# Kernel optimization log

Measured on AMD Instinct MI355X. Metric: run time of the kernel, lower is better.

The kernel has to match this reference:

```python
import jax, jax.numpy as jnp
import numpy as np

B, C, T = 8, 512, 2048
G = 32          # GroupNorm groups
HEADS = 8       # C // head_channels(64)
EPS = 1e-5


def setup_inputs() -> dict:
    key = jax.random.key(0)
    ks = jax.random.split(key, 7)
    s = 0.02
    return {
        "x": jax.random.normal(ks[0], (B, C, T), dtype=jnp.float32),
        "gn_w": jnp.ones((C,), dtype=jnp.float32),
        "gn_b": jnp.zeros((C,), dtype=jnp.float32),
        "qkv_w": jax.random.normal(ks[1], (3 * C, C), dtype=jnp.float32) * s,
        "qkv_b": jnp.zeros((3 * C,), dtype=jnp.float32),
        "proj_w": jax.random.normal(ks[2], (C, C), dtype=jnp.float32) * s,
        "proj_b": jnp.zeros((C,), dtype=jnp.float32),
    }


def reference(x, gn_w, gn_b, qkv_w, qkv_b, proj_w, proj_b):
    b, c, t = x.shape
    ch = c // HEADS
    # GroupNorm(32, C): normalize over (channels-in-group, T)
    xg = x.reshape(b, G, (c // G) * t)
    mu = jnp.mean(xg, axis=-1, keepdims=True)
    var = jnp.var(xg, axis=-1, keepdims=True)
    h = ((xg - mu) * jax.lax.rsqrt(var + EPS)).reshape(b, c, t)
    h = h * gn_w[:, None] + gn_b[:, None]
    # 1x1 Conv1d -> pointwise linear over channels
    qkv = jnp.einsum('oc,bct->bot', qkv_w, h) + qkv_b[:, None]  # [b, 3c, t]
    q, k, v = jnp.split(qkv, 3, axis=1)
    scale = ch ** -0.25
    q = (q * scale).reshape(b * HEADS, ch, t)
    k = (k * scale).reshape(b * HEADS, ch, t)
    v = v.reshape(b * HEADS, ch, t)
    w = jnp.einsum('bct,bcs->bts', q, k)  # [b*H, t, t]
    w = jax.nn.softmax(w.astype(jnp.float32), axis=-1).astype(q.dtype)
    a = jnp.einsum('bts,bcs->bct', w, v).reshape(b, c, t)
    out = jnp.einsum('oc,bct->bot', proj_w, a) + proj_b[:, None]
    return x + out
```

## Files before the change

kernel.cpp:

```cpp
#include <hip/hip_runtime.h>
#include <hip/hip_bf16.h>
#include <math.h>

#define NB 8
#define NC 512
#define NT 2048
#define NG 32
#define NH 8
#define CH 64

typedef __attribute__((ext_vector_type(8))) short short8;
typedef __attribute__((ext_vector_type(4))) short short4v;
typedef __attribute__((ext_vector_type(4))) float floatx4;

static __device__ __forceinline__ short f2bf(float f) {
    __hip_bfloat16 h = __float2bfloat16(f);
    return *reinterpret_cast<short*>(&h);
}

static __device__ __forceinline__ int pk2bf_trunc(float lo, float hi) {
    return (int)__builtin_amdgcn_perm(__builtin_bit_cast(unsigned, hi),
                                      __builtin_bit_cast(unsigned, lo),
                                      0x07060302u);
}

static __device__ __forceinline__ void gload_lds16(const short* g, short* l) {
    __builtin_amdgcn_global_load_lds(
        (const __attribute__((address_space(1))) void*)g,
        (__attribute__((address_space(3))) void*)l, 16, 0, 0);
}

__global__ __launch_bounds__(256) void castw_kernel(
    const float* __restrict__ qw, const float* __restrict__ pw,
    short* __restrict__ qo, short* __restrict__ po)
{
    const int i = blockIdx.x * 256 + threadIdx.x;
    const bool isq = i < 196608;
    const int j = isq ? i : i - 196608;
    float4 v = isq ? ((const float4*)qw)[j] : ((const float4*)pw)[j];
    short4v s;
    s.x = f2bf(v.x); s.y = f2bf(v.y); s.z = f2bf(v.z); s.w = f2bf(v.w);
    if (isq) *(short4v*)&qo[j * 4] = s;
    else     *(short4v*)&po[j * 4] = s;
}

__global__ __launch_bounds__(256) void gn_stats_kernel(
    const float* __restrict__ x, float* __restrict__ stats)
{
    __shared__ float red[16];
    const int tid = threadIdx.x;
    const int grp = blockIdx.x;
    const float4* xp = (const float4*)(x + (size_t)grp * 16 * NT);

    float s = 0.f, ss = 0.f;
    for (int i = tid; i < 8192; i += 256) {
        float4 v = xp[i];
        s  += v.x + v.y + v.z + v.w;
        ss += v.x*v.x + v.y*v.y + v.z*v.z + v.w*v.w;
    }
    #pragma unroll
    for (int o = 32; o > 0; o >>= 1) {
        s  += __shfl_down(s,  o, 64);
        ss += __shfl_down(ss, o, 64);
    }
    const int lane = tid & 63, wid = tid >> 6;
    if (lane == 0) { red[wid] = s; red[8 + wid] = ss; }
    __syncthreads();
    if (tid == 0) {
        const float inv = 1.f / 32768.f;
        const float mean = (red[0] + red[1] + red[2] + red[3]) * inv;
        const float var  = (red[8] + red[9] + red[10] + red[11]) * inv - mean * mean;
        stats[grp * 2]     = mean;
        stats[grp * 2 + 1] = rsqrtf(var + 1e-5f);
    }
}

__global__ __launch_bounds__(256) void gn_apply_kernel(
    const float* __restrict__ x, const float* __restrict__ gw,
    const float* __restrict__ gb, const float* __restrict__ stats,
    short* __restrict__ ht)
{
    __shared__ float wc_s[NC], bc_s[NC];
    __shared__ float tile[64 * 68];
    const int tid = threadIdx.x;
    const int b = blockIdx.y;
    const int t0 = blockIdx.x * 64;

    for (int c = tid; c < NC; c += 256) {
        const int g = c >> 4;
        const float mean = stats[(b * NG + g) * 2];
        const float rstd = stats[(b * NG + g) * 2 + 1];
        const float wc = gw[c] * rstd;
        wc_s[c] = wc;
        bc_s[c] = gb[c] - mean * wc;
    }

    const int cl = tid >> 2;
    const int k4 = tid & 3;
    const int tl = tid >> 2;
    const int cs = (tid & 3) * 16;

    for (int p = 0; p < 8; ++p) {
        const int c0 = p * 64;
        __syncthreads();
        const float* src = x + ((size_t)b * NC + c0 + cl) * NT + t0;
        #pragma unroll
        for (int k = 0; k < 4; ++k) {
            float4 v = *(const float4*)(src + k4 * 16 + k * 4);
            *(float4*)&tile[cl * 68 + k4 * 16 + k * 4] = v;
        }
        __syncthreads();
        short v16[16];
        #pragma unroll
        for (int j = 0; j < 16; ++j) {
            const int c = c0 + cs + j;
            v16[j] = f2bf(tile[(cs + j) * 68 + tl] * wc_s[c] + bc_s[c]);
        }
        short* dst = ht + ((size_t)b * NT + t0 + tl) * NC + c0 + cs;
        *(short8*)&dst[0] = *(const short8*)&v16[0];
        *(short8*)&dst[8] = *(const short8*)&v16[8];
    }
}

#define BK 32
__global__ __launch_bounds__(256) void qkv_gemm_kernel(
    const short* __restrict__ wb, const short* __restrict__ ht,
    const float* __restrict__ bias,
    short* __restrict__ q_t, short* __restrict__ k_t, short* __restrict__ vv)
{
    __shared__ short As[128 * BK];
    __shared__ short Bs[128 * BK];
    const int tid = threadIdx.x;
    const int wv = tid >> 6, lane = tid & 63;
    const int l16 = lane & 15, quad = lane >> 4;
    const int n0 = blockIdx.x * 128;
    const int m0 = blockIdx.y * 128;
    const int wm = wv & 1, wn = wv >> 1;

    floatx4 acc[4][4];
    #pragma unroll
    for (int i = 0; i < 4; ++i)
        #pragma unroll
        for (int j = 0; j < 4; ++j) acc[i][j] = (floatx4){0.f, 0.f, 0.f, 0.f};

    const short* gsrc = (wv < 2) ? wb : ht;
    const int rbase = (wv & 1) * 64;
    const int tile0 = (wv < 2) ? m0 : n0;
    short* lbuf = (wv < 2) ? As : Bs;
    const int lrow = lane >> 2;
    const int lcol = (lane & 3) * 8;

    for (int k0 = 0; k0 < 512; k0 += BK) {
        __syncthreads();
        #pragma unroll
        for (int ch = 0; ch < 4; ++ch) {
            const int row = rbase + ch * 16 + lrow;
            gload_lds16(gsrc + (size_t)(tile0 + row) * 512 + k0 + lcol,
                        lbuf + (rbase + ch * 16) * BK);
        }
        __syncthreads();

        short8 af[4], bfr[4];
        #pragma unroll
        for (int i = 0; i < 4; ++i) {
            af[i]  = *(const short8*)&As[(wm * 64 + i * 16 + l16) * BK + quad * 8];
            bfr[i] = *(const short8*)&Bs[(wn * 64 + i * 16 + l16) * BK + quad * 8];
        }
        #pragma unroll
        for (int i = 0; i < 4; ++i)
            #pragma unroll
            for (int j = 0; j < 4; ++j)
                acc[i][j] = __builtin_amdgcn_mfma_f32_16x16x32_bf16(
                    af[i], bfr[j], acc[i][j], 0, 0, 0);
    }

    const float kscale = 0.35355339059327373f;
    const float qscale = 0.35355339059327373f * 1.4426950408889634f;
    #pragma unroll
    for (int i = 0; i < 4; ++i) {
        const int o16 = m0 + wm * 64 + i * 16;
        const int sel = o16 >> 9;
        const int hh  = (o16 >> 6) & 7;
        const int c16 = o16 & 63;
        const float4 b4 = *(const float4*)&bias[o16 + quad * 4];
        const float sc = (sel == 0) ? qscale : kscale;
        #pragma unroll
        for (int j = 0; j < 4; ++j) {
            const int tg = n0 + wn * 64 + j * 16 + l16;
            const int b = tg >> 11, t = tg & 2047;
            floatx4 v = acc[i][j];
            v[0] += b4.x; v[1] += b4.y; v[2] += b4.z; v[3] += b4.w;
            if (sel < 2) {
                short4v s;
                s.x = f2bf(v[0] * sc); s.y = f2bf(v[1] * sc);
                s.z = f2bf(v[2] * sc); s.w = f2bf(v[3] * sc);
                short* dst = (sel == 0 ? q_t : k_t) +
                    (((size_t)(b * NH + hh) * NT + t) * CH + c16 + quad * 4);
                *(short4v*)dst = s;
            } else {
                short* dst = vv + ((size_t)(b * NH + hh) * CH + c16 + quad * 4) * NT + t;
                #pragma unroll
                for (int r = 0; r < 4; ++r) dst[(size_t)r * NT] = f2bf(v[r]);
            }
        }
    }
}

__global__ __launch_bounds__(512, 4) void attn_kernel(
    const short* __restrict__ qg, const short* __restrict__ kg,
    const short* __restrict__ vg, short* __restrict__ at)
{
    __shared__ short qps[256 * 64];
    __shared__ short kt[2][64 * 64];
    __shared__ short vs[2][64 * 64];

    const int tid = threadIdx.x;
    const int wv = tid >> 6, lane = tid & 63;
    const int l16 = lane & 15, quad = lane >> 4;
    const int xr = l16 & 7;
    const int t0 = blockIdx.x * 256;
    const int bh = blockIdx.y;
    const int b = bh >> 3, hd = bh & 7;
    const short* qh = qg + (size_t)bh * NT * CH;
    const short* kh = kg + (size_t)bh * NT * CH;
    const short* vh = vg + (size_t)bh * CH * NT;

    #pragma unroll
    for (int q = 0; q < 4; ++q) {
        const int F = (wv * 4 + q) * 64 + lane;
        const int row = F >> 3, cc = (F & 7) ^ (row & 7);
        gload_lds16(qh + (size_t)(t0 + row) * CH + cc * 8, &qps[(wv * 4 + q) * 512]);
    }
    {
        const int row = tid >> 3, cc = (tid & 7) ^ (row & 7);
        gload_lds16(kh + (size_t)row * CH + cc * 8, &kt[0][wv * 512]);
        gload_lds16(vh + (size_t)row * NT + cc * 8, &vs[0][wv * 512]);
    }
    __syncthreads();

    short8 bq[2][2];
    #pragma unroll
    for (int qt = 0; qt < 2; ++qt) {
        const int row = wv * 32 + qt * 16 + l16;
        #pragma unroll
        for (int ks = 0; ks < 2; ++ks) {
            const int c = (quad | (ks << 2)) ^ xr;
            bq[qt][ks] = *(const short8*)&qps[row * 64 + c * 8];
        }
    }

    floatx4 Oa[4][2];
    #pragma unroll
    for (int ct = 0; ct < 4; ++ct)
        #pragma unroll
        for (int qt = 0; qt < 2; ++qt) Oa[ct][qt] = (floatx4){0.f, 0.f, 0.f, 0.f};
    float l_part[2] = {0.f, 0.f};

    for (int it = 0; it < NT / 64; ++it) {
        __syncthreads();
        if (it + 1 < NT / 64) {
            const int s0n = (it + 1) * 64;
            const int row = tid >> 3, cc = (tid & 7) ^ (row & 7);
            gload_lds16(kh + (size_t)(s0n + row) * CH + cc * 8,
                        &kt[(it + 1) & 1][wv * 512]);
            gload_lds16(vh + (size_t)row * NT + s0n + cc * 8,
                        &vs[(it + 1) & 1][wv * 512]);
        }
        const short* kc = kt[it & 1];
        const short* vc = vs[it & 1];

        floatx4 sacc[4][2];
        #pragma unroll
        for (int nt = 0; nt < 4; ++nt)
            #pragma unroll
            for (int qt = 0; qt < 2; ++qt) sacc[nt][qt] = (floatx4){0.f, 0.f, 0.f, 0.f};
        #pragma unroll
        for (int ks = 0; ks < 2; ++ks) {
            const int c = (quad | (ks << 2)) ^ xr;
            #pragma unroll
            for (int nt = 0; nt < 4; ++nt) {
                short8 ak = *(const short8*)&kc[(nt * 16 + l16) * 64 + c * 8];
                #pragma unroll
                for (int qt = 0; qt < 2; ++qt)
                    sacc[nt][qt] = __builtin_amdgcn_mfma_f32_16x16x32_bf16(
                        ak, bq[qt][ks], sacc[nt][qt], 0, 0, 0);
            }
        }

        #pragma unroll
        for (int qt = 0; qt < 2; ++qt) {
            float sn[4];
            #pragma unroll
            for (int nt = 0; nt < 4; ++nt) {
                const float p0 = __builtin_amdgcn_exp2f(sacc[nt][qt][0]);
                const float p1 = __builtin_amdgcn_exp2f(sacc[nt][qt][1]);
                const float p2 = __builtin_amdgcn_exp2f(sacc[nt][qt][2]);
                const float p3 = __builtin_amdgcn_exp2f(sacc[nt][qt][3]);
                sacc[nt][qt][0] = p0; sacc[nt][qt][1] = p1;
                sacc[nt][qt][2] = p2; sacc[nt][qt][3] = p3;
                sn[nt] = (p0 + p1) + (p2 + p3);
            }
            l_part[qt] += (sn[0] + sn[1]) + (sn[2] + sn[3]);
        }

        #pragma unroll
        for (int qt = 0; qt < 2; ++qt) {
            const int row = wv * 32 + qt * 16 + l16;
            #pragma unroll
            for (int nt = 0; nt < 4; ++nt) {
                const int cw = (2 * nt + (quad >> 1)) ^ xr;
                int2 pv;
                pv.x = pk2bf_trunc(sacc[nt][qt][0], sacc[nt][qt][1]);
                pv.y = pk2bf_trunc(sacc[nt][qt][2], sacc[nt][qt][3]);
                *(int2*)&qps[row * 64 + cw * 8 + (quad & 1) * 4] = pv;
            }
        }

        #pragma unroll
        for (int ks = 0; ks < 2; ++ks) {
            const int c = (quad | (ks << 2)) ^ xr;
            short8 bp[2];
            #pragma unroll
            for (int qt = 0; qt < 2; ++qt)
                bp[qt] = *(const short8*)&qps[(wv * 32 + qt * 16 + l16) * 64 + c * 8];
            #pragma unroll
            for (int ct = 0; ct < 4; ++ct) {
                short8 av = *(const short8*)&vc[(ct * 16 + l16) * 64 + c * 8];
                #pragma unroll
                for (int qt = 0; qt < 2; ++qt)
                    Oa[ct][qt] = __builtin_amdgcn_mfma_f32_16x16x32_bf16(
                        av, bp[qt], Oa[ct][qt], 0, 0, 0);
            }
        }
    }

    #pragma unroll
    for (int qt = 0; qt < 2; ++qt) {
        float l = l_part[qt];
        l += __shfl_xor(l, 16, 64);
        l += __shfl_xor(l, 32, 64);
        const float rl = 1.f / l;
        const int t = t0 + wv * 32 + qt * 16 + l16;
        short* dst = at + ((size_t)b * NT + t) * NC + hd * CH;
        #pragma unroll
        for (int ct = 0; ct < 4; ++ct) {
            int2 s;
            s.x = pk2bf_trunc(Oa[ct][qt][0] * rl, Oa[ct][qt][1] * rl);
            s.y = pk2bf_trunc(Oa[ct][qt][2] * rl, Oa[ct][qt][3] * rl);
            *(int2*)&dst[ct * 16 + quad * 4] = s;
        }
    }
}

__global__ __launch_bounds__(256) void proj_gemm_kernel(
    const short* __restrict__ wb, const short* __restrict__ at,
    const float* __restrict__ bias, const float* __restrict__ xres,
    float* __restrict__ out)
{
    __shared__ short As[128 * BK];
    __shared__ short Bs[128 * BK];
    const int tid = threadIdx.x;
    const int wv = tid >> 6, lane = tid & 63;
    const int l16 = lane & 15, quad = lane >> 4;
    const int n0 = blockIdx.x * 128;
    const int m0 = blockIdx.y * 128;
    const int wm = wv & 1, wn = wv >> 1;

    floatx4 acc[4][4];
    #pragma unroll
    for (int i = 0; i < 4; ++i)
        #pragma unroll
        for (int j = 0; j < 4; ++j) acc[i][j] = (floatx4){0.f, 0.f, 0.f, 0.f};

    const short* gsrc = (wv < 2) ? wb : at;
    const int rbase = (wv & 1) * 64;
    const int tile0 = (wv < 2) ? m0 : n0;
    short* lbuf = (wv < 2) ? As : Bs;
    const int lrow = lane >> 2;
    const int lcol = (lane & 3) * 8;

    for (int k0 = 0; k0 < 512; k0 += BK) {
        __syncthreads();
        #pragma unroll
        for (int ch = 0; ch < 4; ++ch) {
            const int row = rbase + ch * 16 + lrow;
            gload_lds16(gsrc + (size_t)(tile0 + row) * 512 + k0 + lcol,
                        lbuf + (rbase + ch * 16) * BK);
        }
        __syncthreads();

        short8 af[4], bfr[4];
        #pragma unroll
        for (int i = 0; i < 4; ++i) {
            af[i]  = *(const short8*)&As[(wm * 64 + i * 16 + l16) * BK + quad * 8];
            bfr[i] = *(const short8*)&Bs[(wn * 64 + i * 16 + l16) * BK + quad * 8];
        }
        #pragma unroll
        for (int i = 0; i < 4; ++i)
            #pragma unroll
            for (int j = 0; j < 4; ++j)
                acc[i][j] = __builtin_amdgcn_mfma_f32_16x16x32_bf16(
                    af[i], bfr[j], acc[i][j], 0, 0, 0);
    }

    #pragma unroll
    for (int i = 0; i < 4; ++i) {
        const int o16 = m0 + wm * 64 + i * 16;
        const float4 b4 = *(const float4*)&bias[o16 + quad * 4];
        #pragma unroll
        for (int j = 0; j < 4; ++j) {
            const int tg = n0 + wn * 64 + j * 16 + l16;
            const int b = tg >> 11, t = tg & 2047;
            const size_t base = ((size_t)b * NC + o16 + quad * 4) * NT + t;
            floatx4 v = acc[i][j];
            out[base]          = v[0] + b4.x + xres[base];
            out[base + NT]     = v[1] + b4.y + xres[base + NT];
            out[base + 2 * NT] = v[2] + b4.z + xres[base + 2 * NT];
            out[base + 3 * NT] = v[3] + b4.w + xres[base + 3 * NT];
        }
    }
}

extern "C" void kernel_launch(void* const* d_in, const int* in_sizes, int n_in,
                              void* d_out, int out_size, void* d_ws, size_t ws_size,
                              hipStream_t stream)
{
    const float* x      = (const float*)d_in[0];
    const float* gn_w   = (const float*)d_in[1];
    const float* gn_b   = (const float*)d_in[2];
    const float* qkv_w  = (const float*)d_in[3];
    const float* qkv_b  = (const float*)d_in[4];
    const float* proj_w = (const float*)d_in[5];
    const float* proj_b = (const float*)d_in[6];
    float* out = (float*)d_out;

    short* ht  = (short*)d_ws;
    short* q_t = ht  + 8388608;
    short* k_t = q_t + 8388608;
    short* vv  = k_t + 8388608;
    short* at  = vv  + 8388608;
    short* qwb = at  + 8388608;
    short* pwb = qwb + 786432;
    float* stats = (float*)(pwb + 262144);

    castw_kernel<<<1024, 256, 0, stream>>>(qkv_w, proj_w, qwb, pwb);
    gn_stats_kernel<<<NB * NG, 256, 0, stream>>>(x, stats);
    gn_apply_kernel<<<dim3(NT / 64, NB), 256, 0, stream>>>(x, gn_w, gn_b, stats, ht);
    qkv_gemm_kernel<<<dim3(128, 12), 256, 0, stream>>>(qwb, ht, qkv_b, q_t, k_t, vv);
    attn_kernel<<<dim3(NT / 256, NB * NH), 512, 0, stream>>>(q_t, k_t, vv, at);
    proj_gemm_kernel<<<dim3(128, 4), 256, 0, stream>>>(pwb, at, proj_b, x, out);
}
```

Measured before the change: 261.7 us.

## Keep P in registers via permlane swaps, XCD-aware GEMM block remap, MFMA priority

The attention kernel stops staging Q and the softmax probabilities through shared memory. Q is loaded straight from global into registers, and the bf16-packed P fragments are rearranged into the MFMA B-operand layout with permlane32/permlane16 swaps, removing the LDS write/read round trip and freeing 32KB of LDS. s_setprio hints are placed around the MFMA blocks. Both GEMM kernels remap the flat block index so consecutive N tiles land on the same XCD, aiming for better L2 reuse. The permlane lane mapping has to match the MFMA operand layout exactly, or the results will be wrong.

```diff
diff --git a/kernel.cpp b/kernel.cpp
--- a/kernel.cpp
+++ b/kernel.cpp
@@ -12,6 +12,8 @@
 typedef __attribute__((ext_vector_type(8))) short short8;
 typedef __attribute__((ext_vector_type(4))) short short4v;
 typedef __attribute__((ext_vector_type(4))) float floatx4;
+typedef __attribute__((ext_vector_type(2))) unsigned int uintx2;
+typedef __attribute__((ext_vector_type(4))) unsigned int uintx4;
 
 static __device__ __forceinline__ short f2bf(float f) {
     __hip_bfloat16 h = __float2bfloat16(f);
@@ -133,8 +135,10 @@
     const int tid = threadIdx.x;
     const int wv = tid >> 6, lane = tid & 63;
     const int l16 = lane & 15, quad = lane >> 4;
-    const int n0 = blockIdx.x * 128;
-    const int m0 = blockIdx.y * 128;
+    const int fblk = blockIdx.y * 128 + blockIdx.x;
+    const int jx = fblk >> 3, xcd = fblk & 7;
+    const int n0 = (xcd * 16 + jx / 12) * 128;
+    const int m0 = (jx % 12) * 128;
     const int wm = wv & 1, wn = wv >> 1;
 
     floatx4 acc[4][4];
@@ -210,7 +214,6 @@
     const short* __restrict__ qg, const short* __restrict__ kg,
     const short* __restrict__ vg, short* __restrict__ at)
 {
-    __shared__ short qps[256 * 64];
     __shared__ short kt[2][64 * 64];
     __shared__ short vs[2][64 * 64];
 
@@ -225,29 +228,21 @@
     const short* kh = kg + (size_t)bh * NT * CH;
     const short* vh = vg + (size_t)bh * CH * NT;
 
-    #pragma unroll
-    for (int q = 0; q < 4; ++q) {
-        const int F = (wv * 4 + q) * 64 + lane;
-        const int row = F >> 3, cc = (F & 7) ^ (row & 7);
-        gload_lds16(qh + (size_t)(t0 + row) * CH + cc * 8, &qps[(wv * 4 + q) * 512]);
-    }
     {
         const int row = tid >> 3, cc = (tid & 7) ^ (row & 7);
         gload_lds16(kh + (size_t)row * CH + cc * 8, &kt[0][wv * 512]);
         gload_lds16(vh + (size_t)row * NT + cc * 8, &vs[0][wv * 512]);
     }
+
+    short8 bq[2][2];
+    #pragma unroll
+    for (int qt = 0; qt < 2; ++qt) {
+        const int row = t0 + wv * 32 + qt * 16 + l16;
+        #pragma unroll
+        for (int ks = 0; ks < 2; ++ks)
+            bq[qt][ks] = *(const short8*)&qh[(size_t)row * CH + ks * 32 + quad * 8];
+    }
     __syncthreads();
-
-    short8 bq[2][2];
-    #pragma unroll
-    for (int qt = 0; qt < 2; ++qt) {
-        const int row = wv * 32 + qt * 16 + l16;
-        #pragma unroll
-        for (int ks = 0; ks < 2; ++ks) {
-            const int c = (quad | (ks << 2)) ^ xr;
-            bq[qt][ks] = *(const short8*)&qps[row * 64 + c * 8];
-        }
-    }
 
     floatx4 Oa[4][2];
     #pragma unroll
@@ -274,6 +269,7 @@
         for (int nt = 0; nt < 4; ++nt)
             #pragma unroll
             for (int qt = 0; qt < 2; ++qt) sacc[nt][qt] = (floatx4){0.f, 0.f, 0.f, 0.f};
+        __builtin_amdgcn_s_setprio(1);
         #pragma unroll
         for (int ks = 0; ks < 2; ++ks) {
             const int c = (quad | (ks << 2)) ^ xr;
@@ -286,7 +282,9 @@
                         ak, bq[qt][ks], sacc[nt][qt], 0, 0, 0);
             }
         }
-
+        __builtin_amdgcn_s_setprio(0);
+
+        unsigned pk01[2][4], pk23[2][4];
         #pragma unroll
         for (int qt = 0; qt < 2; ++qt) {
             float sn[4];
@@ -296,33 +294,29 @@
                 const float p1 = __builtin_amdgcn_exp2f(sacc[nt][qt][1]);
                 const float p2 = __builtin_amdgcn_exp2f(sacc[nt][qt][2]);
                 const float p3 = __builtin_amdgcn_exp2f(sacc[nt][qt][3]);
-                sacc[nt][qt][0] = p0; sacc[nt][qt][1] = p1;
-                sacc[nt][qt][2] = p2; sacc[nt][qt][3] = p3;
                 sn[nt] = (p0 + p1) + (p2 + p3);
+                pk01[qt][nt] = (unsigned)pk2bf_trunc(p0, p1);
+                pk23[qt][nt] = (unsigned)pk2bf_trunc(p2, p3);
             }
             l_part[qt] += (sn[0] + sn[1]) + (sn[2] + sn[3]);
         }
 
         #pragma unroll
-        for (int qt = 0; qt < 2; ++qt) {
-            const int row = wv * 32 + qt * 16 + l16;
-            #pragma unroll
-            for (int nt = 0; nt < 4; ++nt) {
-                const int cw = (2 * nt + (quad >> 1)) ^ xr;
-                int2 pv;
-                pv.x = pk2bf_trunc(sacc[nt][qt][0], sacc[nt][qt][1]);
-                pv.y = pk2bf_trunc(sacc[nt][qt][2], sacc[nt][qt][3]);
-                *(int2*)&qps[row * 64 + cw * 8 + (quad & 1) * 4] = pv;
+        for (int ks = 0; ks < 2; ++ks) {
+            short8 bp[2];
+            #pragma unroll
+            for (int qt = 0; qt < 2; ++qt) {
+                uintx2 a = __builtin_amdgcn_permlane32_swap(
+                    pk01[qt][2 * ks], pk01[qt][2 * ks + 1], false, false);
+                uintx2 w02 = __builtin_amdgcn_permlane16_swap(a.x, a.y, false, false);
+                uintx2 c2 = __builtin_amdgcn_permlane32_swap(
+                    pk23[qt][2 * ks], pk23[qt][2 * ks + 1], false, false);
+                uintx2 w13 = __builtin_amdgcn_permlane16_swap(c2.x, c2.y, false, false);
+                uintx4 wi = (uintx4){w02.x, w13.x, w02.y, w13.y};
+                bp[qt] = __builtin_bit_cast(short8, wi);
             }
-        }
-
-        #pragma unroll
-        for (int ks = 0; ks < 2; ++ks) {
             const int c = (quad | (ks << 2)) ^ xr;
-            short8 bp[2];
-            #pragma unroll
-            for (int qt = 0; qt < 2; ++qt)
-                bp[qt] = *(const short8*)&qps[(wv * 32 + qt * 16 + l16) * 64 + c * 8];
+            __builtin_amdgcn_s_setprio(1);
             #pragma unroll
             for (int ct = 0; ct < 4; ++ct) {
                 short8 av = *(const short8*)&vc[(ct * 16 + l16) * 64 + c * 8];
@@ -331,6 +325,7 @@
                     Oa[ct][qt] = __builtin_amdgcn_mfma_f32_16x16x32_bf16(
                         av, bp[qt], Oa[ct][qt], 0, 0, 0);
             }
+            __builtin_amdgcn_s_setprio(0);
         }
     }
 
@@ -362,8 +357,10 @@
     const int tid = threadIdx.x;
     const int wv = tid >> 6, lane = tid & 63;
     const int l16 = lane & 15, quad = lane >> 4;
-    const int n0 = blockIdx.x * 128;
-    const int m0 = blockIdx.y * 128;
+    const int fblk = blockIdx.y * 128 + blockIdx.x;
+    const int jx = fblk >> 3, xcd = fblk & 7;
+    const int n0 = (xcd * 16 + (jx >> 2)) * 128;
+    const int m0 = (jx & 3) * 128;
     const int wm = wv & 1, wn = wv >> 1;
 
     floatx4 acc[4][4];
```

After: 251.9 us. 3.7% less time.
